# Kernel tuning notes

Hardware: AMD Instinct MI355X
Metric: run time of the kernel (lower is better)

The kernel has to match this reference:

```python
import jax, jax.numpy as jnp
import numpy as np

N = 4096        # nodes (cells)
E = 131072      # edges (avg degree 32)
IN = 3000       # input features (genes)
HID = 128       # hidden dim per head
H = 4           # attention heads
LAT = 16        # latent dim
NEG_SLOPE = 0.2 # PyG GATConv leaky_relu slope


def _gat_sparse(x, src, dst, W, a_src, a_dst, b, concat):
    """PyG GATConv on an edge list (src -> dst, softmax grouped by dst)."""
    n = x.shape[0]
    h_, c = a_src.shape
    h = (x @ W).reshape(n, h_, c)                      # [N,H,C]
    e_src = (h * a_src[None]).sum(-1)                  # [N,H]
    e_dst = (h * a_dst[None]).sum(-1)                  # [N,H]
    e = jax.nn.leaky_relu(e_src[src] + e_dst[dst], NEG_SLOPE)  # [E,H]
    m = jax.ops.segment_max(e, dst, num_segments=n)
    ex = jnp.exp(e - m[dst])
    denom = jax.ops.segment_sum(ex, dst, num_segments=n)
    alpha = ex / (denom[dst] + 1e-16)                  # PyG softmax eps
    out = jax.ops.segment_sum(alpha[:, :, None] * h[src], dst, num_segments=n)
    out = out.reshape(n, h_ * c) if concat else out.mean(1)
    return out + b


def _gat_dense(x, W, a_src, a_dst, b, concat):
    """GATConv over the complete graph (the SVD low-rank reconstruction is
    generically fully dense, so to_sparse() keeps all N^2 entries; with
    used_edge_weight=False only the structure matters)."""
    n = x.shape[0]
    h_, c = a_src.shape
    h = (x @ W).reshape(n, h_, c)
    e_src = (h * a_src[None]).sum(-1)                  # [N,H]
    e_dst = (h * a_dst[None]).sum(-1)                  # [N,H]
    # scores[i (target), j (source), head]
    scores = jax.nn.leaky_relu(e_dst[:, None, :] + e_src[None, :, :], NEG_SLOPE)
    alpha = jax.nn.softmax(scores, axis=1)             # softmax over sources
    out = jnp.einsum('ijh,jhc->ihc', alpha, h)
    out = out.reshape(n, h_ * c) if concat else out.mean(1)
    return out + b


def setup_inputs() -> dict:
    key = jax.random.key(0)
    ks = jax.random.split(key, 16)
    s = 0.05
    x = jax.random.normal(ks[0], (N, IN), jnp.float32)
    src = jax.random.randint(ks[1], (E,), 0, N, jnp.int32)
    off = jax.random.randint(ks[2], (E,), 1, N, jnp.int32)
    dst = (src + off) % N                              # no self loops (PyG re-adds them)
    edge_index = jnp.stack([src, dst], axis=0)
    edge_attr = jax.random.uniform(ks[3], (E,), jnp.float32)
    D1 = H * HID
    return {
        'x': x, 'edge_index': edge_index, 'edge_attr': edge_attr,
        'W1': jax.random.normal(ks[4], (IN, D1), jnp.float32) * s,
        'a1_src': jax.random.normal(ks[5], (H, HID), jnp.float32) * s,
        'a1_dst': jax.random.normal(ks[6], (H, HID), jnp.float32) * s,
        'b1': jnp.zeros((D1,), jnp.float32),
        'Wm': jax.random.normal(ks[7], (D1, H * LAT), jnp.float32) * s,
        'am_src': jax.random.normal(ks[8], (H, LAT), jnp.float32) * s,
        'am_dst': jax.random.normal(ks[9], (H, LAT), jnp.float32) * s,
        'bm': jnp.zeros((LAT,), jnp.float32),
        'Ws': jax.random.normal(ks[10], (D1, H * LAT), jnp.float32) * s,
        'as_src': jax.random.normal(ks[11], (H, LAT), jnp.float32) * s,
        'as_dst': jax.random.normal(ks[12], (H, LAT), jnp.float32) * s,
        'bs': jnp.zeros((LAT,), jnp.float32),
    }


def reference(x, edge_index, edge_attr, W1, a1_src, a1_dst, b1,
              Wm, am_src, am_dst, bm, Ws, as_src, as_dst, bs):
    loops = jnp.arange(N, dtype=edge_index.dtype)
    src = jnp.concatenate([edge_index[0], loops])      # GATConv add_self_loops=True
    dst = jnp.concatenate([edge_index[1], loops])
    # branch 1: original sparse graph
    x1 = _gat_sparse(x, src, dst, W1, a1_src, a1_dst, b1, True)
    z_mean1 = _gat_sparse(x1, src, dst, Wm, am_src, am_dst, bm, False)
    z_log_std1 = _gat_sparse(x1, src, dst, Ws, as_src, as_dst, bs, False)
    # branch 2: SVD low-rank reconstructed adjacency => complete graph
    x2 = _gat_dense(x, W1, a1_src, a1_dst, b1, True)
    z_mean2 = _gat_dense(x2, Wm, am_src, am_dst, bm, False)
    z_log_std2 = _gat_dense(x2, Ws, as_src, as_dst, bs, False)
    return (z_mean1, z_log_std1, z_mean2, z_log_std2)
```

## Files before the change

kernel.cpp:

```cpp
#include <hip/hip_runtime.h>

typedef unsigned short u16;
typedef unsigned long long u64;
typedef __attribute__((ext_vector_type(8))) short short8;
typedef __attribute__((ext_vector_type(4))) float f32x4;

#define NN   4096
#define EE   131072
#define ETOT (EE + NN)
#define HH   4
#define IND  3000
#define KP   3008
#define D1   512
#define C1   128
#define C2   16

__device__ __forceinline__ float b2f(u16 u){
  union { unsigned int i; float f; } v; v.i = ((unsigned int)u) << 16; return v.f;
}
__device__ __forceinline__ u16 f2b(float f){
  unsigned int x = __float_as_uint(f);
  unsigned int r = (x + 0x7fffu + ((x >> 16) & 1u)) >> 16;
  return (u16)r;
}
__device__ __forceinline__ float lrelu(float x){ return x > 0.f ? x : 0.2f * x; }

__device__ __forceinline__ void glds16(const void* g, void* l){
  __builtin_amdgcn_global_load_lds(
      (const __attribute__((address_space(1))) unsigned int*)g,
      (__attribute__((address_space(3))) unsigned int*)l, 16, 0, 0);
}

__global__ void zero_out_kernel(float* p, int n){
  int i = blockIdx.x * blockDim.x + threadIdx.x;
  if (i < n) p[i] = 0.f;
}

__global__ __launch_bounds__(256) void cvtXW_kernel(const float* __restrict__ X,
    const float* __restrict__ W, u16* __restrict__ Xhi, u16* __restrict__ Xlo,
    u16* __restrict__ Whi, u16* __restrict__ Wlo){
  __shared__ float T[64][65];
  int b = blockIdx.x;
  if (b < 6016){
    int id = b * 256 + threadIdx.x;
    int m = id / 376, ch = id - m * 376;
    int k = ch * 8;
    float v[8];
    if (k + 8 <= IND){
      float4 a = *(const float4*)(X + (size_t)m * IND + k);
      float4 bb = *(const float4*)(X + (size_t)m * IND + k + 4);
      v[0]=a.x; v[1]=a.y; v[2]=a.z; v[3]=a.w; v[4]=bb.x; v[5]=bb.y; v[6]=bb.z; v[7]=bb.w;
    } else {
      #pragma unroll
      for (int j = 0; j < 8; ++j){ int kk = k + j; v[j] = (kk < IND) ? X[(size_t)m*IND + kk] : 0.f; }
    }
    u16 h8[8], l8[8];
    #pragma unroll
    for (int j = 0; j < 8; ++j){ h8[j] = f2b(v[j]); l8[j] = f2b(v[j] - b2f(h8[j])); }
    *(uint4*)(Xhi + (size_t)m * KP + k) = *(uint4*)h8;
    *(uint4*)(Xlo + (size_t)m * KP + k) = *(uint4*)l8;
  } else {
    int wb = b - 6016;
    int kb = wb % 47, nb = wb / 47;
    int k0 = kb * 64, n0 = nb * 64;
    int t = threadIdx.x;
    #pragma unroll
    for (int rr = 0; rr < 4; ++rr){
      int kl = (t >> 4) + rr * 16;
      int nn = (t & 15) * 4;
      int k = k0 + kl;
      float4 v = make_float4(0.f, 0.f, 0.f, 0.f);
      if (k < IND) v = *(const float4*)(W + (size_t)k * D1 + n0 + nn);
      T[kl][nn] = v.x; T[kl][nn+1] = v.y; T[kl][nn+2] = v.z; T[kl][nn+3] = v.w;
    }
    __syncthreads();
    int nloc = t >> 2, kseg = (t & 3) * 16;
    int n = n0 + nloc;
    #pragma unroll
    for (int c2 = 0; c2 < 2; ++c2){
      int kloc = kseg + c2 * 8;
      u16 h8[8], l8[8];
      #pragma unroll
      for (int j = 0; j < 8; ++j){
        float f = T[kloc + j][nloc];
        h8[j] = f2b(f); l8[j] = f2b(f - b2f(h8[j]));
      }
      *(uint4*)(Whi + (size_t)n * KP + k0 + kloc) = *(uint4*)h8;
      *(uint4*)(Wlo + (size_t)n * KP + k0 + kloc) = *(uint4*)l8;
    }
  }
}

__global__ __launch_bounds__(256) void cvtW2_kernel(const float* __restrict__ WM,
    const float* __restrict__ WS, u16* __restrict__ Wh, u16* __restrict__ Wl){
  __shared__ float T[64][65];
  int half = blockIdx.y;
  int k0 = blockIdx.x * 64;
  const float* W = half ? WS : WM;
  int t = threadIdx.x;
  #pragma unroll
  for (int p = 0; p < 4; ++p){
    int r = p * 16 + (t >> 4), c4 = (t & 15) * 4;
    float4 v = *(const float4*)(W + (size_t)(k0 + r) * 64 + c4);
    T[r][c4] = v.x; T[r][c4+1] = v.y; T[r][c4+2] = v.z; T[r][c4+3] = v.w;
  }
  __syncthreads();
  #pragma unroll
  for (int p = 0; p < 4; ++p){
    int n = p * 16 + (t >> 4), k4 = (t & 15) * 4;
    u16 h4[4], l4[4];
    #pragma unroll
    for (int j = 0; j < 4; ++j){
      float f = T[k4 + j][n];
      h4[j] = f2b(f); l4[j] = f2b(f - b2f(h4[j]));
    }
    size_t o = (size_t)(half * 64 + n) * 512 + k0 + k4;
    *(ushort4*)(Wh + o) = *(ushort4*)h4;
    *(ushort4*)(Wl + o) = *(ushort4*)l4;
  }
}

__global__ __launch_bounds__(512) void gemm_mfma(const u16* __restrict__ Xhi,
    const u16* __restrict__ Xlo, const u16* __restrict__ Whi, const u16* __restrict__ Wlo,
    float* __restrict__ Hh){
  __shared__ u16 sbuf[2][4][4096];
  int t = threadIdx.x, lane = t & 63;
  int wv = __builtin_amdgcn_readfirstlane(t >> 6);
  int ksw = wv >> 2;
  int wr = (wv >> 1) & 1, wc = wv & 1;
  int bm = blockIdx.x * 64, bn = blockIdx.y * 64;
  f32x4 acc[2][2] = {};
  int srow = t >> 3;
  int sc = (t & 7) ^ (srow & 7);
  const char* gAh = (const char*)(Xhi + (size_t)(bm + srow) * KP) + sc * 16;
  const char* gAl = (const char*)(Xlo + (size_t)(bm + srow) * KP) + sc * 16;
  const char* gBh = (const char*)(Whi + (size_t)(bn + srow) * KP) + sc * 16;
  const char* gBl = (const char*)(Wlo + (size_t)(bn + srow) * KP) + sc * 16;
  int r16 = lane & 15, kq = lane >> 4;
  int cc = ksw * 4 + kq;
  int aoff[2], boff[2];
  #pragma unroll
  for (int m = 0; m < 2; ++m){
    int arow = wr * 32 + m * 16 + r16;
    aoff[m] = arow * 128 + ((cc ^ (arow & 7)) * 16);
  }
  #pragma unroll
  for (int n = 0; n < 2; ++n){
    int brow = wc * 32 + n * 16 + r16;
    boff[n] = brow * 128 + ((cc ^ (brow & 7)) * 16);
  }

  #define STAGE(step, b) do { int ko = (step) * 128;            \
      glds16(gAh + ko, (char*)sbuf[b][0] + t * 16);             \
      glds16(gAl + ko, (char*)sbuf[b][1] + t * 16);             \
      glds16(gBh + ko, (char*)sbuf[b][2] + t * 16);             \
      glds16(gBl + ko, (char*)sbuf[b][3] + t * 16);             \
    } while (0)
  #define BARRIER()  asm volatile("s_barrier" ::: "memory")
  #define WAIT_V4()  asm volatile("s_waitcnt vmcnt(4)" ::: "memory")
  #define WAIT_V0()  asm volatile("s_waitcnt vmcnt(0)" ::: "memory")

  STAGE(0, 0);
  STAGE(1, 1);
  WAIT_V4();
  BARRIER();
  for (int i = 0; i < 47; ++i){
    int cur = i & 1;
    const char* pAh = (const char*)sbuf[cur][0];
    const char* pAl = (const char*)sbuf[cur][1];
    const char* pBh = (const char*)sbuf[cur][2];
    const char* pBl = (const char*)sbuf[cur][3];
    short8 ah[2], al[2], bh[2], bl[2];
    #pragma unroll
    for (int m = 0; m < 2; ++m){
      ah[m] = *(const short8*)(pAh + aoff[m]);
      al[m] = *(const short8*)(pAl + aoff[m]);
    }
    #pragma unroll
    for (int n = 0; n < 2; ++n){
      bh[n] = *(const short8*)(pBh + boff[n]);
      bl[n] = *(const short8*)(pBl + boff[n]);
    }
    #pragma unroll
    for (int m = 0; m < 2; ++m)
      #pragma unroll
      for (int n = 0; n < 2; ++n){
        acc[m][n] = __builtin_amdgcn_mfma_f32_16x16x32_bf16(ah[m], bh[n], acc[m][n], 0, 0, 0);
        acc[m][n] = __builtin_amdgcn_mfma_f32_16x16x32_bf16(ah[m], bl[n], acc[m][n], 0, 0, 0);
        acc[m][n] = __builtin_amdgcn_mfma_f32_16x16x32_bf16(al[m], bh[n], acc[m][n], 0, 0, 0);
      }
    BARRIER();
    if (i + 2 < 47){
      STAGE(i + 2, cur);
      WAIT_V4();
    } else {
      WAIT_V0();
    }
    BARRIER();
  }
  #undef STAGE
  #undef BARRIER
  #undef WAIT_V4
  #undef WAIT_V0
  float* red = (float*)sbuf;
  int pp = wr * 2 + wc;
  if (ksw){
    #pragma unroll
    for (int m = 0; m < 2; ++m)
      #pragma unroll
      for (int n = 0; n < 2; ++n)
        #pragma unroll
        for (int r = 0; r < 4; ++r)
          red[((((m*2+n)*4 + r) << 8) + (pp << 6)) + lane] = acc[m][n][r];
  }
  __syncthreads();
  if (!ksw){
    #pragma unroll
    for (int m = 0; m < 2; ++m)
      #pragma unroll
      for (int n = 0; n < 2; ++n){
        #pragma unroll
        for (int r = 0; r < 4; ++r)
          acc[m][n][r] += red[((((m*2+n)*4 + r) << 8) + (pp << 6)) + lane];
        int row = bm + wr * 32 + m * 16 + kq * 4;
        int col = bn + wc * 32 + n * 16 + r16;
        float* o = Hh + (size_t)row * D1 + col;
        #pragma unroll
        for (int r = 0; r < 4; ++r) o[(size_t)r * D1] = acc[m][n][r];
      }
  }
}

__global__ __launch_bounds__(256) void gemm_h_split(const float* __restrict__ X,
    const float* __restrict__ Wc, float* __restrict__ Hh){
  __shared__ u16 Ahs[64][40], Als[64][40], Bhs[64][40], Bls[64][40];
  int t = threadIdx.x, lane = t & 63, wave = t >> 6;
  int wr = wave >> 1, wcc = wave & 1;
  int bm = blockIdx.x * 64, bn = blockIdx.y * 64;
  f32x4 acc[2][2] = {};
  int arow = t >> 2, akc = (t & 3) << 3;
  int brow = t >> 3, bnc = (t & 7) << 3;
  for (int k0 = 0; k0 < IND; k0 += 32){
    float va[8];
    size_t abase = (size_t)(bm + arow) * IND + k0 + akc;
    if (k0 + akc + 8 <= IND){
      float4 r0 = *(const float4*)(X + abase);
      float4 r1 = *(const float4*)(X + abase + 4);
      va[0]=r0.x; va[1]=r0.y; va[2]=r0.z; va[3]=r0.w;
      va[4]=r1.x; va[5]=r1.y; va[6]=r1.z; va[7]=r1.w;
    } else {
      #pragma unroll
      for (int j = 0; j < 8; ++j){
        int k = k0 + akc + j;
        va[j] = (k < IND) ? X[abase + j] : 0.f;
      }
    }
    #pragma unroll
    for (int j = 0; j < 8; ++j){
      u16 hb = f2b(va[j]);
      Ahs[arow][akc + j] = hb;
      Als[arow][akc + j] = f2b(va[j] - b2f(hb));
    }
    {
      int gk = k0 + brow;
      float vb[8];
      if (gk < IND){
        const float* wp = Wc + (size_t)gk * D1 + bn + bnc;
        float4 r0 = *(const float4*)wp;
        float4 r1 = *(const float4*)(wp + 4);
        vb[0]=r0.x; vb[1]=r0.y; vb[2]=r0.z; vb[3]=r0.w;
        vb[4]=r1.x; vb[5]=r1.y; vb[6]=r1.z; vb[7]=r1.w;
      } else {
        #pragma unroll
        for (int j = 0; j < 8; ++j) vb[j] = 0.f;
      }
      #pragma unroll
      for (int j = 0; j < 8; ++j){
        u16 hb = f2b(vb[j]);
        Bhs[bnc + j][brow] = hb;
        Bls[bnc + j][brow] = f2b(vb[j] - b2f(hb));
      }
    }
    __syncthreads();
    int r16 = lane & 15, kq = (lane >> 4) << 3;
    short8 a0h = *(const short8*)&Ahs[wr*32      + r16][kq];
    short8 a1h = *(const short8*)&Ahs[wr*32 + 16 + r16][kq];
    short8 a0l = *(const short8*)&Als[wr*32      + r16][kq];
    short8 a1l = *(const short8*)&Als[wr*32 + 16 + r16][kq];
    short8 b0h = *(const short8*)&Bhs[wcc*32      + r16][kq];
    short8 b1h = *(const short8*)&Bhs[wcc*32 + 16 + r16][kq];
    short8 b0l = *(const short8*)&Bls[wcc*32      + r16][kq];
    short8 b1l = *(const short8*)&Bls[wcc*32 + 16 + r16][kq];
    acc[0][0] = __builtin_amdgcn_mfma_f32_16x16x32_bf16(a0h, b0h, acc[0][0], 0, 0, 0);
    acc[0][1] = __builtin_amdgcn_mfma_f32_16x16x32_bf16(a0h, b1h, acc[0][1], 0, 0, 0);
    acc[1][0] = __builtin_amdgcn_mfma_f32_16x16x32_bf16(a1h, b0h, acc[1][0], 0, 0, 0);
    acc[1][1] = __builtin_amdgcn_mfma_f32_16x16x32_bf16(a1h, b1h, acc[1][1], 0, 0, 0);
    acc[0][0] = __builtin_amdgcn_mfma_f32_16x16x32_bf16(a0h, b0l, acc[0][0], 0, 0, 0);
    acc[0][1] = __builtin_amdgcn_mfma_f32_16x16x32_bf16(a0h, b1l, acc[0][1], 0, 0, 0);
    acc[1][0] = __builtin_amdgcn_mfma_f32_16x16x32_bf16(a1h, b0l, acc[1][0], 0, 0, 0);
    acc[1][1] = __builtin_amdgcn_mfma_f32_16x16x32_bf16(a1h, b1l, acc[1][1], 0, 0, 0);
    acc[0][0] = __builtin_amdgcn_mfma_f32_16x16x32_bf16(a0l, b0h, acc[0][0], 0, 0, 0);
    acc[0][1] = __builtin_amdgcn_mfma_f32_16x16x32_bf16(a0l, b1h, acc[0][1], 0, 0, 0);
    acc[1][0] = __builtin_amdgcn_mfma_f32_16x16x32_bf16(a1l, b0h, acc[1][0], 0, 0, 0);
    acc[1][1] = __builtin_amdgcn_mfma_f32_16x16x32_bf16(a1l, b1h, acc[1][1], 0, 0, 0);
    __syncthreads();
  }
  int cr = (lane >> 4) << 2, cc = lane & 15;
  for (int i = 0; i < 2; ++i) for (int j = 0; j < 2; ++j){
    int row = bm + wr*32 + i*16 + cr;
    int col = bn + wcc*32 + j*16 + cc;
    float* o = Hh + (size_t)row * D1 + col;
    for (int r = 0; r < 4; ++r) o[(size_t)r * D1] = acc[i][j][r];
  }
}

__global__ __launch_bounds__(256) void transpose_h(const float* __restrict__ h,
    float* __restrict__ hT, u16* __restrict__ h16){
  __shared__ float T[64][65];
  int bm = blockIdx.x * 64, bc = blockIdx.y * 64;
  int t = threadIdx.x;
  #pragma unroll
  for (int p = 0; p < 4; ++p){
    int r = p * 16 + (t >> 4), c4 = (t & 15) * 4;
    float4 v = *(const float4*)(h + (size_t)(bm + r) * D1 + bc + c4);
    T[r][c4] = v.x; T[r][c4+1] = v.y; T[r][c4+2] = v.z; T[r][c4+3] = v.w;
    u16 q[4] = { f2b(v.x), f2b(v.y), f2b(v.z), f2b(v.w) };
    *(ushort4*)(h16 + (size_t)(bm + r) * D1 + bc + c4) = *(ushort4*)q;
  }
  __syncthreads();
  #pragma unroll
  for (int p = 0; p < 4; ++p){
    int c = p * 16 + (t >> 4), m4 = (t & 15) * 4;
    float4 o = make_float4(T[m4][c], T[m4+1][c], T[m4+2][c], T[m4+3][c]);
    *(float4*)(hT + (size_t)(bc + c) * NN + bm + m4) = o;
  }
}

__global__ __launch_bounds__(256) void evec128(const float* __restrict__ hsrc,
    const float* __restrict__ as_, const float* __restrict__ ad_,
    float* __restrict__ es, float* __restrict__ ed){
  int idx = blockIdx.x * 256 + threadIdx.x;
  if (idx >= NN * HH) return;
  int h = idx & 3;
  const float4* hp = (const float4*)(hsrc + (size_t)idx * C1);
  const float4* ap = (const float4*)(as_ + h * C1);
  const float4* dp = (const float4*)(ad_ + h * C1);
  float s1 = 0.f, s2 = 0.f;
  #pragma unroll
  for (int c = 0; c < 32; ++c){
    float4 v = hp[c], a = ap[c], d = dp[c];
    s1 += v.x*a.x + v.y*a.y + v.z*a.z + v.w*a.w;
    s2 += v.x*d.x + v.y*d.y + v.z*d.z + v.w*d.w;
  }
  es[idx] = s1; ed[idx] = s2;
}

__global__ void zero_kernel(int* p, int n){
  int i = blockIdx.x * blockDim.x + threadIdx.x;
  if (i < n) p[i] = 0;
}
__global__ void hist_kernel(const int* __restrict__ dstA, int* __restrict__ deg){
  int e = blockIdx.x * blockDim.x + threadIdx.x;
  if (e < ETOT){
    int d = (e < EE) ? dstA[e] : (e - EE);
    atomicAdd(&deg[d & (NN-1)], 1);
  }
}
__global__ __launch_bounds__(1024) void scan_kernel(const int* __restrict__ deg,
    int* __restrict__ off, int* __restrict__ cur){
  __shared__ int wsum[16];
  int t = threadIdx.x, lane = t & 63, wv = t >> 6;
  int v0 = deg[t*4], v1 = deg[t*4+1], v2 = deg[t*4+2], v3 = deg[t*4+3];
  int s = v0 + v1 + v2 + v3;
  int sc = s;
  #pragma unroll
  for (int o = 1; o < 64; o <<= 1){
    int y = __shfl_up(sc, o);
    if (lane >= o) sc += y;
  }
  if (lane == 63) wsum[wv] = sc;
  __syncthreads();
  int base = 0;
  #pragma unroll
  for (int i = 0; i < 16; ++i) base += (i < wv) ? wsum[i] : 0;
  int excl = base + sc - s;
  int a0 = excl, a1 = a0 + v0, a2 = a1 + v1, a3 = a2 + v2;
  off[t*4] = a0; off[t*4+1] = a1; off[t*4+2] = a2; off[t*4+3] = a3;
  cur[t*4] = a0; cur[t*4+1] = a1; cur[t*4+2] = a2; cur[t*4+3] = a3;
  if (t == 1023) off[4096] = base + sc;
}
__global__ void scatter_kernel(const int* __restrict__ srcA, const int* __restrict__ dstA,
    int* __restrict__ cur, int* __restrict__ sidx){
  int e = blockIdx.x * blockDim.x + threadIdx.x;
  if (e < ETOT){
    int s, d;
    if (e < EE){ s = srcA[e]; d = dstA[e]; } else { s = d = e - EE; }
    int pos = atomicAdd(&cur[d & (NN-1)], 1);
    pos = min(max(pos, 0), ETOT - 1);
    sidx[pos] = s & (NN-1);
  }
}

__global__ __launch_bounds__(256) void sparse1(const u16* __restrict__ h16,
    const float* __restrict__ es, const float* __restrict__ ed,
    const int* __restrict__ off, const int* __restrict__ sidx,
    const float* __restrict__ bias, u16* __restrict__ x1h, u16* __restrict__ x1l){
  int n = blockIdx.x, t = threadIdx.x, w = t >> 6;
  int o0 = off[n], deg = off[n+1] - o0;
  deg = min(max(deg, 0), ETOT);
  float edn = ed[n * HH + w];
  float dsum = 1e-16f, a0 = 0.f, a1 = 0.f;
  for (int e = 0; e < deg; ++e){
    int s = sidx[o0 + e] & (NN-1);
    float we = __expf(lrelu(es[s*HH + w] + edn));
    unsigned pk = *(const unsigned*)(h16 + ((size_t)s << 9) + 2*t);
    a0 = fmaf(we, b2f((u16)(pk & 0xffff)), a0);
    a1 = fmaf(we, b2f((u16)(pk >> 16)), a1);
    dsum += we;
  }
  float inv = 1.0f / dsum;
  float v0 = a0 * inv + bias[2*t];
  float v1 = a1 * inv + bias[2*t + 1];
  u16 h0 = f2b(v0), h1 = f2b(v1);
  u16 l0 = f2b(v0 - b2f(h0)), l1 = f2b(v1 - b2f(h1));
  size_t o = ((size_t)n << 9) + 2*t;
  *(unsigned*)(x1h + o) = (unsigned)h0 | ((unsigned)h1 << 16);
  *(unsigned*)(x1l + o) = (unsigned)l0 | ((unsigned)l1 << 16);
}

struct Sp2 { const float* h[2]; const float* es[2]; const float* ed[2];
             const float* bias[2]; float* out[2]; };
__global__ __launch_bounds__(64) void sparse2(Sp2 a,
    const int* __restrict__ off, const int* __restrict__ sidx){
  int n = blockIdx.x, sel = blockIdx.y;
  int lane = threadIdx.x, hh = lane >> 4;
  const float* hsrc = a.h[sel];
  const float* es = a.es[sel];
  const float* ed = a.ed[sel];
  int o0 = off[n], deg = off[n+1] - o0;
  deg = min(max(deg, 0), ETOT);
  float edn = ed[n * HH + hh];
  float dsum = 1e-16f, acc = 0.f;
  for (int e = 0; e < deg; ++e){
    int s = sidx[o0 + e] & (NN-1);
    float we = __expf(lrelu(es[s*HH + hh] + edn));
    acc = fmaf(we, hsrc[(size_t)s * 64 + lane], acc);
    dsum += we;
  }
  float v = acc / dsum;
  v += __shfl_xor(v, 16);
  v += __shfl_xor(v, 32);
  if (lane < 16) a.out[sel][(size_t)n * C2 + lane] = v * 0.25f + a.bias[sel][lane];
}

struct GsA {
  const u16* x1h; const u16* x1l; const u16* x2h; const u16* x2l;
  const u16* Wh; const u16* Wl;
  float* hm1; float* hs1; float* hm2T; float* hs2T;
  const float* AMS; const float* AMD; const float* ASS; const float* ASD;
  float* em1s; float* em1d; float* es1s; float* es1d;
  float* em2s; float* em2d; float* es2s; float* es2d;
};
__global__ __launch_bounds__(256) void gemm_small_fused(GsA a){
  __shared__ u16 sAh[32*64], sAl[32*64], sBh[128*64], sBl[128*64];
  int t = threadIdx.x, lane = t & 63;
  int wv = __builtin_amdgcn_readfirstlane(t >> 6);
  int src = blockIdx.y;
  int bm = blockIdx.x * 32;
  const u16* xh = src ? a.x2h : a.x1h;
  const u16* xl = src ? a.x2l : a.x1l;
  f32x4 acc[2][2] = {};
  int sarow = t >> 3, sac = (t & 7) ^ (sarow & 7);
  const char* gAh = (const char*)(xh + (size_t)(bm + sarow) * 512) + sac * 16;
  const char* gAl = (const char*)(xl + (size_t)(bm + sarow) * 512) + sac * 16;
  char* lAh = (char*)sAh + t * 16;
  char* lAl = (char*)sAl + t * 16;
  const char* gBh[4]; const char* gBl[4];
  #pragma unroll
  for (int q = 0; q < 4; ++q){
    int id = q * 256 + t;
    int br = id >> 3, bc = (id & 7) ^ (br & 7);
    gBh[q] = (const char*)(a.Wh + (size_t)br * 512) + bc * 16;
    gBl[q] = (const char*)(a.Wl + (size_t)br * 512) + bc * 16;
  }
  int r16 = lane & 15, kq = lane >> 4;
  int aoff[2][2], boff[2][2];
  #pragma unroll
  for (int m = 0; m < 2; ++m)
    #pragma unroll
    for (int ks = 0; ks < 2; ++ks){
      int arow = m * 16 + r16;
      int cc = ks * 4 + kq;
      aoff[m][ks] = arow * 128 + ((cc ^ (arow & 7)) * 16);
    }
  #pragma unroll
  for (int n = 0; n < 2; ++n)
    #pragma unroll
    for (int ks = 0; ks < 2; ++ks){
      int brow = wv * 32 + n * 16 + r16;
      int cc = ks * 4 + kq;
      boff[n][ks] = brow * 128 + ((cc ^ (brow & 7)) * 16);
    }
  for (int kb = 0; kb < 1024; kb += 128){
    glds16(gAh + kb, lAh);
    glds16(gAl + kb, lAl);
    #pragma unroll
    for (int q = 0; q < 4; ++q){
      glds16(gBh[q] + kb, (char*)sBh + (q * 256 + t) * 16);
      glds16(gBl[q] + kb, (char*)sBl + (q * 256 + t) * 16);
    }
    __syncthreads();
    #pragma unroll
    for (int ks = 0; ks < 2; ++ks){
      short8 ah[2], al[2], bh[2], bl[2];
      #pragma unroll
      for (int m = 0; m < 2; ++m){
        ah[m] = *(const short8*)((const char*)sAh + aoff[m][ks]);
        al[m] = *(const short8*)((const char*)sAl + aoff[m][ks]);
      }
      #pragma unroll
      for (int n = 0; n < 2; ++n){
        bh[n] = *(const short8*)((const char*)sBh + boff[n][ks]);
        bl[n] = *(const short8*)((const char*)sBl + boff[n][ks]);
      }
      #pragma unroll
      for (int m = 0; m < 2; ++m)
        #pragma unroll
        for (int n = 0; n < 2; ++n){
          acc[m][n] = __builtin_amdgcn_mfma_f32_16x16x32_bf16(ah[m], bh[n], acc[m][n], 0, 0, 0);
          acc[m][n] = __builtin_amdgcn_mfma_f32_16x16x32_bf16(ah[m], bl[n], acc[m][n], 0, 0, 0);
          acc[m][n] = __builtin_amdgcn_mfma_f32_16x16x32_bf16(al[m], bh[n], acc[m][n], 0, 0, 0);
        }
    }
    __syncthreads();
  }
  #pragma unroll
  for (int m = 0; m < 2; ++m){
    #pragma unroll
    for (int n = 0; n < 2; ++n){
      int colB = wv * 32 + n * 16;
      int half = colB >> 6;
      int colh = (colB & 63) + r16;
      int hh = (colB & 63) >> 4;
      int row0 = bm + m * 16 + kq * 4;
      if (src == 0){
        float* o = (half ? a.hs1 : a.hm1) + (size_t)row0 * 64 + colh;
        #pragma unroll
        for (int r = 0; r < 4; ++r) o[(size_t)r * 64] = acc[m][n][r];
      } else {
        float* oT = (half ? a.hs2T : a.hm2T) + (size_t)colh * NN + row0;
        *(float4*)oT = make_float4(acc[m][n][0], acc[m][n][1], acc[m][n][2], acc[m][n][3]);
      }
      const float* AS = half ? a.ASS : a.AMS;
      const float* AD = half ? a.ASD : a.AMD;
      float av = AS[colh], dv = AD[colh];
      float* esP = src ? (half ? a.es2s : a.em2s) : (half ? a.es1s : a.em1s);
      float* edP = src ? (half ? a.es2d : a.em2d) : (half ? a.es1d : a.em1d);
      #pragma unroll
      for (int r = 0; r < 4; ++r){
        float vs = acc[m][n][r] * av;
        float vd = acc[m][n][r] * dv;
        #pragma unroll
        for (int msk = 1; msk < 16; msk <<= 1){
          vs += __shfl_xor(vs, msk);
          vd += __shfl_xor(vd, msk);
        }
        if (r16 == 0){
          int rw = row0 + r;
          esP[rw * HH + hh] = vs;
          edP[rw * HH + hh] = vd;
        }
      }
    }
  }
}

struct RkA { const float* in[2]; float* us[2]; int* pm[2]; };
__global__ __launch_bounds__(1024) void rank_kernel(RkA a){
  int sid = blockIdx.y;
  int sel = sid >> 2, h = sid & 3;
  const float* evals = a.in[sel];
  __shared__ u64 K[NN];
  __shared__ int red[1024];
  int t = threadIdx.x;
  for (int i = t; i < NN; i += 1024){
    unsigned x = __float_as_uint(evals[i*HH + h]);
    x = (x & 0x80000000u) ? ~x : (x | 0x80000000u);
    K[i] = ((u64)x << 32) | (unsigned)i;
  }
  __syncthreads();
  int jl = t & 63, sp = t >> 6;
  int j = blockIdx.x * 64 + jl;
  u64 myk = K[j];
  int cnt = 0;
  int k0 = sp * 256;
  #pragma unroll 8
  for (int i = 0; i < 256; ++i)
    cnt += (K[k0 + i] < myk) ? 1 : 0;
  red[t] = cnt;
  __syncthreads();
  if (sp == 0){
    int rank = 0;
    #pragma unroll
    for (int s = 0; s < 16; ++s) rank += red[jl + 64*s];
    a.us[sel][h*NN + rank] = evals[j*HH + h];
    a.pm[sel][h*NN + rank] = j;
  }
}

struct PfxA { const float* T[2]; const int* pm[2]; const float* us[2];
              float* P1[2]; float* P2[2]; };
__global__ __launch_bounds__(512) void prefix_kernel(PfxA a, int C){
  int sel = blockIdx.y;
  int Cp = C + 1;
  int h = blockIdx.x / Cp, c = blockIdx.x % Cp;
  const float* Tsrc = a.T[sel];
  const int*   pm   = a.pm[sel] + h * NN;
  const float* us   = a.us[sel] + h * NN;
  float* P1 = a.P1[sel];
  float* P2 = a.P2[sel];
  const float* row = Tsrc + (size_t)(h * C + c) * NN;
  __shared__ float L1[NN], L2[NN];
  __shared__ float T1[8], T2[8], O1[9], O2[9];
  int t = threadIdx.x, lane = t & 63, w = t >> 6;
  size_t base = (size_t)h * (NN + 1);
  float run1 = 0.f, run2 = 0.f;
  for (int cc = 0; cc < 8; ++cc){
    int k = w * 512 + cc * 64 + lane;
    float u = us[k];
    float v = 1.0f;
    if (c < C){ int j = pm[k] & (NN-1); v = row[j]; }
    float t1 = __expf(u) * v;
    float t2 = __expf(0.2f * u) * v;
    float s1 = t1, s2 = t2;
    for (int o = 1; o < 64; o <<= 1){
      float y1 = __shfl_up(s1, o), y2 = __shfl_up(s2, o);
      if (lane >= o){ s1 += y1; s2 += y2; }
    }
    L1[k] = run1 + s1 - t1;
    L2[k] = run2 + s2 - t2;
    run1 += __shfl(s1, 63);
    run2 += __shfl(s2, 63);
  }
  if (lane == 63){ T1[w] = run1; T2[w] = run2; }
  __syncthreads();
  if (t == 0){
    float a1 = 0.f, a2 = 0.f;
    #pragma unroll
    for (int s = 0; s < 8; ++s){ O1[s] = a1; O2[s] = a2; a1 += T1[s]; a2 += T2[s]; }
    O1[8] = a1; O2[8] = a2;
  }
  __syncthreads();
  for (int i = t; i < NN; i += 512){
    P1[(base + i) * Cp + c] = L1[i] + O1[i >> 9];
    P2[(base + i) * Cp + c] = L2[i] + O2[i >> 9];
  }
  if (t == 0){
    P1[(base + NN) * Cp + c] = O1[8];
    P2[(base + NN) * Cp + c] = O2[8];
  }
}

template<int C, bool MEAN>
__device__ __forceinline__ void dense_body(const float* __restrict__ P1,
    const float* __restrict__ P2, const float* __restrict__ usort,
    const float* __restrict__ ed, const float* __restrict__ bias,
    float* __restrict__ outF, u16* __restrict__ outH, u16* __restrict__ outL, int i){
  constexpr int Cp = C + 1;
  constexpr int NC = HH * C;
  int t = threadIdx.x;
  __shared__ float Ed[HH], E2d[HH], Den[HH];
  __shared__ int   Kh[HH];
  __shared__ float vals[NC > 256 ? 1 : NC];
  if (t < HH){
    float d = ed[i*HH + t];
    float target = -d;
    const float* us = usort + t * NN;
    int lo = 0, hi = NN;
    while (lo < hi){ int mid = (lo + hi) >> 1; if (us[mid] < target) lo = mid + 1; else hi = mid; }
    Kh[t] = lo;
    float e1 = __expf(d), e2 = __expf(0.2f * d);
    Ed[t] = e1; E2d[t] = e2;
    size_t base = (size_t)t * (NN + 1);
    float p1N = P1[(base + NN) * Cp + C];
    float p1k = P1[(base + lo) * Cp + C];
    float p2k = P2[(base + lo) * Cp + C];
    Den[t] = e1 * (p1N - p1k) + e2 * p2k;
  }
  __syncthreads();
  if (!MEAN){
    for (int ch = t; ch < NC; ch += 256){
      int h = ch / C, c = ch % C;
      size_t base = (size_t)h * (NN + 1);
      float p1N = P1[(base + NN)    * Cp + c];
      float p1k = P1[(base + Kh[h]) * Cp + c];
      float p2k = P2[(base + Kh[h]) * Cp + c];
      float num = Ed[h] * (p1N - p1k) + E2d[h] * p2k;
      float val = num / Den[h] + bias[ch];
      u16 hb = f2b(val);
      outH[(size_t)i * NC + ch] = hb;
      outL[(size_t)i * NC + ch] = f2b(val - b2f(hb));
    }
  } else {
    if (t < NC){
      int h = t / C, c = t % C;
      size_t base = (size_t)h * (NN + 1);
      float p1N = P1[(base + NN)    * Cp + c];
      float p1k = P1[(base + Kh[h]) * Cp + c];
      float p2k = P2[(base + Kh[h]) * Cp + c];
      vals[t] = (Ed[h] * (p1N - p1k) + E2d[h] * p2k) / Den[h];
    }
    __syncthreads();
    if (t < C){
      float z = (vals[t] + vals[C + t] + vals[2*C + t] + vals[3*C + t]) * 0.25f + bias[t];
      outF[(size_t)i * C + t] = z;
    }
  }
}

__global__ __launch_bounds__(256) void dense_out1(const float* __restrict__ P1,
    const float* __restrict__ P2, const float* __restrict__ usort,
    const float* __restrict__ ed, const float* __restrict__ bias,
    u16* __restrict__ outH, u16* __restrict__ outL){
  dense_body<C1, false>(P1, P2, usort, ed, bias, nullptr, outH, outL, blockIdx.x);
}

struct Dn2 { const float* P1[2]; const float* P2[2]; const float* us[2];
             const float* ed[2]; const float* bias[2]; float* out[2]; };
__global__ __launch_bounds__(256) void dense_out2(Dn2 a){
  int s = blockIdx.y;
  dense_body<C2, true>(a.P1[s], a.P2[s], a.us[s], a.ed[s], a.bias[s], a.out[s],
                       nullptr, nullptr, blockIdx.x);
}

extern "C" void kernel_launch(void* const* d_in, const int* in_sizes, int n_in,
                              void* d_out, int out_size, void* d_ws, size_t ws_size,
                              hipStream_t stream){
  const float* X   = (const float*)d_in[0];
  const int*   EI  = (const int*)d_in[1];
  const float* W1  = (const float*)d_in[3];
  const float* A1S = (const float*)d_in[4];
  const float* A1D = (const float*)d_in[5];
  const float* B1  = (const float*)d_in[6];
  const float* WM  = (const float*)d_in[7];
  const float* AMS = (const float*)d_in[8];
  const float* AMD = (const float*)d_in[9];
  const float* BM  = (const float*)d_in[10];
  const float* WS  = (const float*)d_in[11];
  const float* ASS = (const float*)d_in[12];
  const float* ASD = (const float*)d_in[13];
  const float* BS  = (const float*)d_in[14];
  float* OUT = (float*)d_out;
  (void)in_sizes; (void)n_in;

  if (ws_size < (size_t)56 * 1024 * 1024){
    zero_out_kernel<<<dim3((out_size + 255)/256), 256, 0, stream>>>(OUT, out_size);
    return;
  }
  bool fast = (ws_size >= (size_t)68 * 1024 * 1024);

  const size_t MB = 1024 * 1024;
  char* w = (char*)d_ws;
  size_t o = 0;
  auto alloc = [&](size_t bytes) -> void* {
    void* p = w + o;
    o += (bytes + 255) & ~(size_t)255;
    return p;
  };
  int*   deg  = (int*)  alloc(NN * 4);
  int*   coff = (int*)  alloc((NN + 1) * 4);
  int*   cur  = (int*)  alloc(NN * 4);
  int*   sidx = (int*)  alloc((size_t)ETOT * 4);
  float* e1s  = (float*)alloc(NN * HH * 4);
  float* e1d  = (float*)alloc(NN * HH * 4);
  float* us1  = (float*)alloc(HH * NN * 4);
  int*   pm1  = (int*)  alloc(HH * NN * 4);
  float* em1s = (float*)alloc(NN * HH * 4);
  float* em1d = (float*)alloc(NN * HH * 4);
  float* es1s = (float*)alloc(NN * HH * 4);
  float* es1d = (float*)alloc(NN * HH * 4);
  float* em2s = (float*)alloc(NN * HH * 4);
  float* em2d = (float*)alloc(NN * HH * 4);
  float* es2s = (float*)alloc(NN * HH * 4);
  float* es2d = (float*)alloc(NN * HH * 4);
  float* us2m = (float*)alloc(HH * NN * 4);
  int*   pm2m = (int*)  alloc(HH * NN * 4);
  float* us2s = (float*)alloc(HH * NN * 4);
  int*   pm2s = (int*)  alloc(HH * NN * 4);
  u16*   Wh2  = (u16*)  alloc(128 * 512 * 2);
  u16*   Wl2  = (u16*)  alloc(128 * 512 * 2);
  float* h    = (float*)alloc((size_t)NN * D1 * 4);
  char*  BIG  = w + o;
  size_t szX = (size_t)NN * KP * 2, szW = (size_t)D1 * KP * 2;
  u16* Xhi = (u16*)BIG;
  u16* Xlo = (u16*)(BIG + szX);
  u16* Whi = (u16*)(BIG + 2*szX);
  u16* Wlo = (u16*)(BIG + 2*szX + szW);
  u16*   x1h = (u16*)  (BIG + 0*MB);
  u16*   x1l = (u16*)  (BIG + 4*MB);
  u16*   x2h = (u16*)  (BIG + 8*MB);
  u16*   x2l = (u16*)  (BIG + 12*MB);
  float* hT  = (float*)(BIG + 16*MB);
  u16*   h16 = (u16*)  (BIG + 24*MB);
  float* P1a = (float*)(BIG + 28*MB);
  float* P2a = (float*)(BIG + 37*MB);
  float* hm1  = (float*)(BIG + 16*MB);
  float* hs1  = (float*)(BIG + 17*MB);
  float* hm2T = (float*)(BIG + 18*MB);
  float* hs2T = (float*)(BIG + 19*MB);
  float* P1m  = (float*)(BIG + 20*MB);
  float* P2m  = (float*)(BIG + 21*MB + 512*1024);
  float* P1s  = (float*)(BIG + 23*MB);
  float* P2s  = (float*)(BIG + 24*MB + 512*1024);

  const int* srcA = EI;
  const int* dstA = EI + EE;

  cvtW2_kernel<<<dim3(8, 2), 256, 0, stream>>>(WM, WS, Wh2, Wl2);
  if (fast){
    cvtXW_kernel<<<dim3(6016 + 47*8), 256, 0, stream>>>(X, W1, Xhi, Xlo, Whi, Wlo);
    gemm_mfma<<<dim3(NN/64, D1/64), 512, 0, stream>>>(Xhi, Xlo, Whi, Wlo, h);
  } else {
    gemm_h_split<<<dim3(NN/64, D1/64), 256, 0, stream>>>(X, W1, h);
  }
  transpose_h<<<dim3(NN/64, D1/64), 256, 0, stream>>>(h, hT, h16);
  evec128<<<dim3(NN*HH/256), 256, 0, stream>>>(h, A1S, A1D, e1s, e1d);
  zero_kernel<<<dim3(16), 256, 0, stream>>>(deg, NN);
  hist_kernel<<<dim3((ETOT + 255)/256), 256, 0, stream>>>(dstA, deg);
  scan_kernel<<<dim3(1), 1024, 0, stream>>>(deg, coff, cur);
  scatter_kernel<<<dim3((ETOT + 255)/256), 256, 0, stream>>>(srcA, dstA, cur, sidx);
  sparse1<<<dim3(NN), 256, 0, stream>>>(h16, e1s, e1d, coff, sidx, B1, x1h, x1l);
  {
    RkA ra; ra.in[0] = e1s; ra.in[1] = e1s; ra.us[0] = us1; ra.us[1] = us1;
    ra.pm[0] = pm1; ra.pm[1] = pm1;
    rank_kernel<<<dim3(64, 4), 1024, 0, stream>>>(ra);
    PfxA pa; pa.T[0] = hT; pa.T[1] = hT; pa.pm[0] = pm1; pa.pm[1] = pm1;
    pa.us[0] = us1; pa.us[1] = us1; pa.P1[0] = P1a; pa.P1[1] = P1a;
    pa.P2[0] = P2a; pa.P2[1] = P2a;
    prefix_kernel<<<dim3(HH*(C1+1), 1), 512, 0, stream>>>(pa, C1);
    dense_out1<<<dim3(NN), 256, 0, stream>>>(P1a, P2a, us1, e1d, B1, x2h, x2l);
  }
  {
    GsA ga;
    ga.x1h = x1h; ga.x1l = x1l; ga.x2h = x2h; ga.x2l = x2l;
    ga.Wh = Wh2; ga.Wl = Wl2;
    ga.hm1 = hm1; ga.hs1 = hs1; ga.hm2T = hm2T; ga.hs2T = hs2T;
    ga.AMS = AMS; ga.AMD = AMD; ga.ASS = ASS; ga.ASD = ASD;
    ga.em1s = em1s; ga.em1d = em1d; ga.es1s = es1s; ga.es1d = es1d;
    ga.em2s = em2s; ga.em2d = em2d; ga.es2s = es2s; ga.es2d = es2d;
    gemm_small_fused<<<dim3(NN/32, 2), 256, 0, stream>>>(ga);
  }
  {
    Sp2 sp;
    sp.h[0] = hm1; sp.h[1] = hs1; sp.es[0] = em1s; sp.es[1] = es1s;
    sp.ed[0] = em1d; sp.ed[1] = es1d; sp.bias[0] = BM; sp.bias[1] = BS;
    sp.out[0] = OUT; sp.out[1] = OUT + (size_t)NN*C2;
    sparse2<<<dim3(NN, 2), 64, 0, stream>>>(sp, coff, sidx);
  }
  {
    RkA ra; ra.in[0] = em2s; ra.in[1] = es2s; ra.us[0] = us2m; ra.us[1] = us2s;
    ra.pm[0] = pm2m; ra.pm[1] = pm2s;
    rank_kernel<<<dim3(64, 8), 1024, 0, stream>>>(ra);
    PfxA pa; pa.T[0] = hm2T; pa.T[1] = hs2T; pa.pm[0] = pm2m; pa.pm[1] = pm2s;
    pa.us[0] = us2m; pa.us[1] = us2s; pa.P1[0] = P1m; pa.P1[1] = P1s;
    pa.P2[0] = P2m; pa.P2[1] = P2s;
    prefix_kernel<<<dim3(HH*(C2+1), 2), 512, 0, stream>>>(pa, C2);
    Dn2 dn;
    dn.P1[0] = P1m; dn.P1[1] = P1s; dn.P2[0] = P2m; dn.P2[1] = P2s;
    dn.us[0] = us2m; dn.us[1] = us2s; dn.ed[0] = em2d; dn.ed[1] = es2d;
    dn.bias[0] = BM; dn.bias[1] = BS;
    dn.out[0] = OUT + (size_t)2*NN*C2; dn.out[1] = OUT + (size_t)3*NN*C2;
    dense_out2<<<dim3(NN, 2), 256, 0, stream>>>(dn);
  }
}
```

Baseline: 380.6 us.

## Replace single-pass prefix kernel with three-phase chunked scan and drop transposes

The per-column prefix scan over sorted sources, which ran as one block per (head, channel) and needed a transposed copy of h, is split into three phases: chunk totals, a scan across chunk totals, and an emit pass that writes running prefixes while re-reading h in row-major form. The h transpose kernel becomes a plain bf16 conversion, and the small GEMM writes its outputs row-major instead of transposed. This exposes more parallelism across chunks and removes transpose traffic, at the cost of two extra launches, gathered row reads of h, and the intermediate T buffers.

```diff
diff --git a/kernel.cpp b/kernel.cpp
--- a/kernel.cpp
+++ b/kernel.cpp
@@ -314,26 +314,14 @@
   }
 }
 
-__global__ __launch_bounds__(256) void transpose_h(const float* __restrict__ h,
-    float* __restrict__ hT, u16* __restrict__ h16){
-  __shared__ float T[64][65];
-  int bm = blockIdx.x * 64, bc = blockIdx.y * 64;
-  int t = threadIdx.x;
-  #pragma unroll
-  for (int p = 0; p < 4; ++p){
-    int r = p * 16 + (t >> 4), c4 = (t & 15) * 4;
-    float4 v = *(const float4*)(h + (size_t)(bm + r) * D1 + bc + c4);
-    T[r][c4] = v.x; T[r][c4+1] = v.y; T[r][c4+2] = v.z; T[r][c4+3] = v.w;
-    u16 q[4] = { f2b(v.x), f2b(v.y), f2b(v.z), f2b(v.w) };
-    *(ushort4*)(h16 + (size_t)(bm + r) * D1 + bc + c4) = *(ushort4*)q;
-  }
-  __syncthreads();
-  #pragma unroll
-  for (int p = 0; p < 4; ++p){
-    int c = p * 16 + (t >> 4), m4 = (t & 15) * 4;
-    float4 o = make_float4(T[m4][c], T[m4+1][c], T[m4+2][c], T[m4+3][c]);
-    *(float4*)(hT + (size_t)(bc + c) * NN + bm + m4) = o;
-  }
+__global__ __launch_bounds__(256) void cvt_h16(const float* __restrict__ h,
+    u16* __restrict__ h16){
+  size_t i = ((size_t)blockIdx.x * 256 + threadIdx.x) * 8;
+  float4 va = *(const float4*)(h + i);
+  float4 vb = *(const float4*)(h + i + 4);
+  u16 q[8] = { f2b(va.x), f2b(va.y), f2b(va.z), f2b(va.w),
+               f2b(vb.x), f2b(vb.y), f2b(vb.z), f2b(vb.w) };
+  *(uint4*)(h16 + i) = *(uint4*)q;
 }
 
 __global__ __launch_bounds__(256) void evec128(const float* __restrict__ hsrc,
@@ -456,7 +444,7 @@
 struct GsA {
   const u16* x1h; const u16* x1l; const u16* x2h; const u16* x2l;
   const u16* Wh; const u16* Wl;
-  float* hm1; float* hs1; float* hm2T; float* hs2T;
+  float* hm1; float* hs1; float* hm2; float* hs2;
   const float* AMS; const float* AMD; const float* ASS; const float* ASD;
   float* em1s; float* em1d; float* es1s; float* es1d;
   float* em2s; float* em2d; float* es2s; float* es2d;
@@ -543,14 +531,10 @@
       int colh = (colB & 63) + r16;
       int hh = (colB & 63) >> 4;
       int row0 = bm + m * 16 + kq * 4;
-      if (src == 0){
-        float* o = (half ? a.hs1 : a.hm1) + (size_t)row0 * 64 + colh;
-        #pragma unroll
-        for (int r = 0; r < 4; ++r) o[(size_t)r * 64] = acc[m][n][r];
-      } else {
-        float* oT = (half ? a.hs2T : a.hm2T) + (size_t)colh * NN + row0;
-        *(float4*)oT = make_float4(acc[m][n][0], acc[m][n][1], acc[m][n][2], acc[m][n][3]);
-      }
+      float* o = (src ? (half ? a.hs2 : a.hm2) : (half ? a.hs1 : a.hm1))
+                 + (size_t)row0 * 64 + colh;
+      #pragma unroll
+      for (int r = 0; r < 4; ++r) o[(size_t)r * 64] = acc[m][n][r];
       const float* AS = half ? a.ASS : a.AMS;
       const float* AD = half ? a.ASD : a.AMD;
       float av = AS[colh], dv = AD[colh];
@@ -608,56 +592,124 @@
   }
 }
 
-struct PfxA { const float* T[2]; const int* pm[2]; const float* us[2];
-              float* P1[2]; float* P2[2]; };
-__global__ __launch_bounds__(512) void prefix_kernel(PfxA a, int C){
+struct PfxN { const float* hsrc[2]; const int* pm[2]; const float* us[2];
+              float* T1; float* T2; float* P1[2]; float* P2[2]; };
+
+template<int C, int CW, int G, int KPER, int NCH>
+__global__ __launch_bounds__(512) void pfx_tot(PfxN a){
+  constexpr int Cp = C + 1;
+  constexpr int CHUNK = G * KPER;
+  constexpr int L = G * NCH;
+  __shared__ float E1[CHUNK], E2[CHUNK];
+  __shared__ int PM[CHUNK];
   int sel = blockIdx.y;
-  int Cp = C + 1;
-  int h = blockIdx.x / Cp, c = blockIdx.x % Cp;
-  const float* Tsrc = a.T[sel];
-  const int*   pm   = a.pm[sel] + h * NN;
-  const float* us   = a.us[sel] + h * NN;
+  int h = blockIdx.x / NCH, ch = blockIdx.x % NCH;
+  int tid = threadIdx.x;
+  const float* us = a.us[sel] + h * NN + ch * CHUNK;
+  const int* pm = a.pm[sel] + h * NN + ch * CHUNK;
+  for (int tt = tid; tt < CHUNK; tt += 512){
+    float u = us[tt];
+    E1[tt] = __expf(u); E2[tt] = __expf(0.2f * u);
+    PM[tt] = pm[tt] & (NN - 1);
+  }
+  __syncthreads();
+  int g = tid / C, c = tid % C;
+  const float* hs = a.hsrc[sel];
+  float s1 = 0.f, s2 = 0.f, d1 = 0.f, d2 = 0.f;
+  #pragma unroll
+  for (int j = 0; j < KPER; ++j){
+    int kk = g * KPER + j;
+    float v = hs[(size_t)PM[kk] * CW + h * C + c];
+    s1 = fmaf(E1[kk], v, s1); s2 = fmaf(E2[kk], v, s2);
+    d1 += E1[kk]; d2 += E2[kk];
+  }
+  int pos = ch * G + g;
+  size_t col = (size_t)(sel * HH + h) * Cp + c;
+  a.T1[col * L + pos] = s1;
+  a.T2[col * L + pos] = s2;
+  if (c == 0){
+    size_t colD = (size_t)(sel * HH + h) * Cp + C;
+    a.T1[colD * L + pos] = d1;
+    a.T2[colD * L + pos] = d2;
+  }
+}
+
+template<int C>
+__global__ __launch_bounds__(64) void pfx_scan(PfxN a, int L){
+  constexpr int Cp = C + 1;
+  int sel = blockIdx.y;
+  int col = blockIdx.x;
+  int h = col / Cp, c = col % Cp;
+  size_t gcol = (size_t)(sel * HH + h) * Cp + c;
+  int lane = threadIdx.x;
+  float run1 = 0.f, run2 = 0.f;
+  for (int p0 = 0; p0 < L; p0 += 64){
+    size_t idx = gcol * (size_t)L + p0 + lane;
+    float o1 = a.T1[idx], o2 = a.T2[idx];
+    float a1 = o1, a2 = o2;
+    #pragma unroll
+    for (int o = 1; o < 64; o <<= 1){
+      float y1 = __shfl_up(a1, o), y2 = __shfl_up(a2, o);
+      if (lane >= o){ a1 += y1; a2 += y2; }
+    }
+    a.T1[idx] = run1 + a1 - o1;
+    a.T2[idx] = run2 + a2 - o2;
+    run1 += __shfl(a1, 63);
+    run2 += __shfl(a2, 63);
+  }
+  if (lane == 0){
+    size_t base = (size_t)h * (NN + 1);
+    a.P1[sel][(base + NN) * Cp + c] = run1;
+    a.P2[sel][(base + NN) * Cp + c] = run2;
+  }
+}
+
+template<int C, int CW, int G, int KPER, int NCH>
+__global__ __launch_bounds__(512) void pfx_emit(PfxN a){
+  constexpr int Cp = C + 1;
+  constexpr int CHUNK = G * KPER;
+  constexpr int L = G * NCH;
+  __shared__ float E1[CHUNK], E2[CHUNK];
+  __shared__ int PM[CHUNK];
+  int sel = blockIdx.y;
+  int h = blockIdx.x / NCH, ch = blockIdx.x % NCH;
+  int tid = threadIdx.x;
+  const float* us = a.us[sel] + h * NN + ch * CHUNK;
+  const int* pm = a.pm[sel] + h * NN + ch * CHUNK;
+  for (int tt = tid; tt < CHUNK; tt += 512){
+    float u = us[tt];
+    E1[tt] = __expf(u); E2[tt] = __expf(0.2f * u);
+    PM[tt] = pm[tt] & (NN - 1);
+  }
+  __syncthreads();
+  int g = tid / C, c = tid % C;
+  const float* hs = a.hsrc[sel];
   float* P1 = a.P1[sel];
   float* P2 = a.P2[sel];
-  const float* row = Tsrc + (size_t)(h * C + c) * NN;
-  __shared__ float L1[NN], L2[NN];
-  __shared__ float T1[8], T2[8], O1[9], O2[9];
-  int t = threadIdx.x, lane = t & 63, w = t >> 6;
-  size_t base = (size_t)h * (NN + 1);
-  float run1 = 0.f, run2 = 0.f;
-  for (int cc = 0; cc < 8; ++cc){
-    int k = w * 512 + cc * 64 + lane;
-    float u = us[k];
-    float v = 1.0f;
-    if (c < C){ int j = pm[k] & (NN-1); v = row[j]; }
-    float t1 = __expf(u) * v;
-    float t2 = __expf(0.2f * u) * v;
-    float s1 = t1, s2 = t2;
-    for (int o = 1; o < 64; o <<= 1){
-      float y1 = __shfl_up(s1, o), y2 = __shfl_up(s2, o);
-      if (lane >= o){ s1 += y1; s2 += y2; }
-    }
-    L1[k] = run1 + s1 - t1;
-    L2[k] = run2 + s2 - t2;
-    run1 += __shfl(s1, 63);
-    run2 += __shfl(s2, 63);
-  }
-  if (lane == 63){ T1[w] = run1; T2[w] = run2; }
-  __syncthreads();
-  if (t == 0){
-    float a1 = 0.f, a2 = 0.f;
-    #pragma unroll
-    for (int s = 0; s < 8; ++s){ O1[s] = a1; O2[s] = a2; a1 += T1[s]; a2 += T2[s]; }
-    O1[8] = a1; O2[8] = a2;
-  }
-  __syncthreads();
-  for (int i = t; i < NN; i += 512){
-    P1[(base + i) * Cp + c] = L1[i] + O1[i >> 9];
-    P2[(base + i) * Cp + c] = L2[i] + O2[i >> 9];
-  }
-  if (t == 0){
-    P1[(base + NN) * Cp + c] = O1[8];
-    P2[(base + NN) * Cp + c] = O2[8];
+  int pos = ch * G + g;
+  size_t col = (size_t)(sel * HH + h) * Cp + c;
+  float r1 = a.T1[col * L + pos];
+  float r2 = a.T2[col * L + pos];
+  float rD1 = 0.f, rD2 = 0.f;
+  if (c == 0){
+    size_t colD = (size_t)(sel * HH + h) * Cp + C;
+    rD1 = a.T1[colD * L + pos];
+    rD2 = a.T2[colD * L + pos];
+  }
+  size_t hb = (size_t)h * (NN + 1) + ch * CHUNK + g * KPER;
+  #pragma unroll
+  for (int j = 0; j < KPER; ++j){
+    int kk = g * KPER + j;
+    float v = hs[(size_t)PM[kk] * CW + h * C + c];
+    P1[(hb + j) * Cp + c] = r1;
+    P2[(hb + j) * Cp + c] = r2;
+    r1 = fmaf(E1[kk], v, r1);
+    r2 = fmaf(E2[kk], v, r2);
+    if (c == 0){
+      P1[(hb + j) * Cp + C] = rD1;
+      P2[(hb + j) * Cp + C] = rD2;
+      rD1 += E1[kk]; rD2 += E2[kk];
+    }
   }
 }
 
@@ -800,18 +852,21 @@
   u16*   x1l = (u16*)  (BIG + 4*MB);
   u16*   x2h = (u16*)  (BIG + 8*MB);
   u16*   x2l = (u16*)  (BIG + 12*MB);
-  float* hT  = (float*)(BIG + 16*MB);
+  float* T1a = (float*)(BIG + 16*MB);
+  float* T2a = (float*)(BIG + 17*MB);
   u16*   h16 = (u16*)  (BIG + 24*MB);
   float* P1a = (float*)(BIG + 28*MB);
   float* P2a = (float*)(BIG + 37*MB);
   float* hm1  = (float*)(BIG + 16*MB);
   float* hs1  = (float*)(BIG + 17*MB);
-  float* hm2T = (float*)(BIG + 18*MB);
-  float* hs2T = (float*)(BIG + 19*MB);
+  float* hm2  = (float*)(BIG + 18*MB);
+  float* hs2  = (float*)(BIG + 19*MB);
   float* P1m  = (float*)(BIG + 20*MB);
   float* P2m  = (float*)(BIG + 21*MB + 512*1024);
   float* P1s  = (float*)(BIG + 23*MB);
   float* P2s  = (float*)(BIG + 24*MB + 512*1024);
+  float* T1b  = (float*)(BIG + 26*MB);
+  float* T2b  = (float*)(BIG + 26*MB + 512*1024);
 
   const int* srcA = EI;
   const int* dstA = EI + EE;
@@ -823,7 +878,7 @@
   } else {
     gemm_h_split<<<dim3(NN/64, D1/64), 256, 0, stream>>>(X, W1, h);
   }
-  transpose_h<<<dim3(NN/64, D1/64), 256, 0, stream>>>(h, hT, h16);
+  cvt_h16<<<dim3(1024), 256, 0, stream>>>(h, h16);
   evec128<<<dim3(NN*HH/256), 256, 0, stream>>>(h, A1S, A1D, e1s, e1d);
   zero_kernel<<<dim3(16), 256, 0, stream>>>(deg, NN);
   hist_kernel<<<dim3((ETOT + 255)/256), 256, 0, stream>>>(dstA, deg);
@@ -834,17 +889,23 @@
     RkA ra; ra.in[0] = e1s; ra.in[1] = e1s; ra.us[0] = us1; ra.us[1] = us1;
     ra.pm[0] = pm1; ra.pm[1] = pm1;
     rank_kernel<<<dim3(64, 4), 1024, 0, stream>>>(ra);
-    PfxA pa; pa.T[0] = hT; pa.T[1] = hT; pa.pm[0] = pm1; pa.pm[1] = pm1;
-    pa.us[0] = us1; pa.us[1] = us1; pa.P1[0] = P1a; pa.P1[1] = P1a;
+    PfxN pa;
+    pa.hsrc[0] = h;  pa.hsrc[1] = h;
+    pa.pm[0] = pm1;  pa.pm[1] = pm1;
+    pa.us[0] = us1;  pa.us[1] = us1;
+    pa.T1 = T1a; pa.T2 = T2a;
+    pa.P1[0] = P1a; pa.P1[1] = P1a;
     pa.P2[0] = P2a; pa.P2[1] = P2a;
-    prefix_kernel<<<dim3(HH*(C1+1), 1), 512, 0, stream>>>(pa, C1);
+    pfx_tot<C1, D1, 4, 16, 64><<<dim3(HH*64, 1), 512, 0, stream>>>(pa);
+    pfx_scan<C1><<<dim3(HH*(C1+1), 1), 64, 0, stream>>>(pa, 256);
+    pfx_emit<C1, D1, 4, 16, 64><<<dim3(HH*64, 1), 512, 0, stream>>>(pa);
     dense_out1<<<dim3(NN), 256, 0, stream>>>(P1a, P2a, us1, e1d, B1, x2h, x2l);
   }
   {
     GsA ga;
     ga.x1h = x1h; ga.x1l = x1l; ga.x2h = x2h; ga.x2l = x2l;
     ga.Wh = Wh2; ga.Wl = Wl2;
-    ga.hm1 = hm1; ga.hs1 = hs1; ga.hm2T = hm2T; ga.hs2T = hs2T;
+    ga.hm1 = hm1; ga.hs1 = hs1; ga.hm2 = hm2; ga.hs2 = hs2;
     ga.AMS = AMS; ga.AMD = AMD; ga.ASS = ASS; ga.ASD = ASD;
     ga.em1s = em1s; ga.em1d = em1d; ga.es1s = es1s; ga.es1d = es1d;
     ga.em2s = em2s; ga.em2d = em2d; ga.es2s = es2s; ga.es2d = es2d;
@@ -861,10 +922,16 @@
     RkA ra; ra.in[0] = em2s; ra.in[1] = es2s; ra.us[0] = us2m; ra.us[1] = us2s;
     ra.pm[0] = pm2m; ra.pm[1] = pm2s;
     rank_kernel<<<dim3(64, 8), 1024, 0, stream>>>(ra);
-    PfxA pa; pa.T[0] = hm2T; pa.T[1] = hs2T; pa.pm[0] = pm2m; pa.pm[1] = pm2s;
-    pa.us[0] = us2m; pa.us[1] = us2s; pa.P1[0] = P1m; pa.P1[1] = P1s;
+    PfxN pa;
+    pa.hsrc[0] = hm2; pa.hsrc[1] = hs2;
+    pa.pm[0] = pm2m;  pa.pm[1] = pm2s;
+    pa.us[0] = us2m;  pa.us[1] = us2s;
+    pa.T1 = T1b; pa.T2 = T2b;
+    pa.P1[0] = P1m; pa.P1[1] = P1s;
     pa.P2[0] = P2m; pa.P2[1] = P2s;
-    prefix_kernel<<<dim3(HH*(C2+1), 2), 512, 0, stream>>>(pa, C2);
+    pfx_tot<C2, 64, 32, 8, 16><<<dim3(HH*16, 2), 512, 0, stream>>>(pa);
+    pfx_scan<C2><<<dim3(HH*(C2+1), 2), 64, 0, stream>>>(pa, 512);
+    pfx_emit<C2, 64, 32, 8, 16><<<dim3(HH*16, 2), 512, 0, stream>>>(pa);
     Dn2 dn;
     dn.P1[0] = P1m; dn.P1[1] = P1s; dn.P2[0] = P2m; dn.P2[1] = P2s;
     dn.us[0] = us2m; dn.us[1] = us2s; dn.ed[0] = em2d; dn.ed[1] = es2d;
```

Measured after the change: 353.3 us. 7.2% less time.
